# Optimization experiments

Hardware: AMD Instinct MI355X
Metric: run time of the kernel (lower is better)

The kernel has to match this reference:

```python
import jax, jax.numpy as jnp
import numpy as np

N = 100000   # nodes
E = 1600000  # edges
D_IN = 128
D = 128
G = 64       # graphs in batch
C = 2        # out_channels
EPS = 1e-5   # BatchNorm eps


def setup_inputs() -> dict:
    key = jax.random.key(0)
    ks = jax.random.split(key, 24)
    s = 0.05
    inp = {
        "x": jax.random.normal(ks[0], (N, D_IN), dtype=jnp.float32),
        "edge_index": jax.random.randint(ks[1], (2, E), 0, N, dtype=jnp.int32),
        "edge_attr": jax.random.uniform(ks[2], (E, 2), dtype=jnp.float32),
        "batch": jnp.sort(jax.random.randint(ks[3], (N,), 0, G, dtype=jnp.int32)),
        # GCN layer 0
        "Wg0": jax.random.normal(ks[4], (D_IN, D), dtype=jnp.float32) * s,
        "bg0": jnp.zeros((D,), jnp.float32),
        "gamma0": jnp.ones((D,), jnp.float32),
        "beta0": jnp.zeros((D,), jnp.float32),
        # GCN layer 1
        "Wg1": jax.random.normal(ks[5], (D, D), dtype=jnp.float32) * s,
        "bg1": jnp.zeros((D,), jnp.float32),
        "gamma1": jnp.ones((D,), jnp.float32),
        "beta1": jnp.zeros((D,), jnp.float32),
        # dense head
        "Wl1": jax.random.normal(ks[6], (D, D), dtype=jnp.float32) * s,
        "bl1": jnp.zeros((D,), jnp.float32),
        "Wl2": jax.random.normal(ks[7], (D, D), dtype=jnp.float32) * s,
        "bl2": jnp.zeros((D,), jnp.float32),
        "Wc1": jax.random.normal(ks[8], (D, D), dtype=jnp.float32) * s,
        "bc1": jnp.zeros((D,), jnp.float32),
        "Wc2": jax.random.normal(ks[9], (D, C), dtype=jnp.float32) * s,
        "bc2": jnp.zeros((C,), jnp.float32),
    }
    return inp


def _gcn_conv(x, src, dst, w, W, b):
    # PyG GCNConv: h = x @ W ; add self-loops (weight 1) ; symmetric norm ; agg at dst ; + bias
    h = x @ W                                                   # [N, D]
    deg = jax.ops.segment_sum(w, dst, num_segments=N) + 1.0     # self-loop weight 1
    dinv = jnp.where(deg > 0, jax.lax.rsqrt(deg), 0.0)          # deg^{-1/2}
    norm = dinv[src] * w * dinv[dst]                            # [E]
    agg = jax.ops.segment_sum(norm[:, None] * h[src], dst, num_segments=N)
    agg = agg + (dinv * dinv)[:, None] * h                      # self-loop contribution
    return agg + b


def _bn(x, gamma, beta):
    # training-mode batch statistics over the node dimension
    m = x.mean(axis=0)
    v = x.var(axis=0)
    return (x - m) * jax.lax.rsqrt(v + EPS) * gamma + beta


def reference(x, edge_index, edge_attr, batch,
              Wg0, bg0, gamma0, beta0,
              Wg1, bg1, gamma1, beta1,
              Wl1, bl1, Wl2, bl2, Wc1, bc1, Wc2, bc2):
    src, dst = edge_index[0], edge_index[1]
    w = edge_attr[:, 1]  # which_edge_weight is None -> column 1

    h = jax.nn.relu(_gcn_conv(x, src, dst, w, Wg0, bg0))
    h = _bn(h, gamma0, beta0)                 # dropout: identity (eval)
    h = jax.nn.relu(_gcn_conv(h, src, dst, w, Wg1, bg1))
    h = _bn(h, gamma1, beta1)

    h = jax.nn.relu(h @ Wl1 + bl1)
    h = h @ Wl2 + bl2                          # node embeddings [N, D]

    counts = jax.ops.segment_sum(jnp.ones((N,), h.dtype), batch, num_segments=G)
    graph_reps = jax.ops.segment_sum(h, batch, num_segments=G) / jnp.maximum(counts, 1.0)[:, None]

    logits = jax.nn.relu(graph_reps @ Wc1 + bc1) @ Wc2 + bc2   # [G, C]
    return (h, graph_reps, logits)
```

## Files before the change

### kernel.cpp

```cpp
#include <hip/hip_runtime.h>

#define N_NODES 100000
#define N_EDGES 1600000
#define DFEAT   128
#define NGRAPH  64
#define EPSV    1e-5f
#define SCAN_BLOCKS ((N_NODES + 255) / 256)
#define DEG_SCALE 268435456.0f
#define DEG_MASK  ((1ULL << 42) - 1)

typedef float v4f  __attribute__((ext_vector_type(4)));
typedef short v8s  __attribute__((ext_vector_type(8)));
typedef unsigned short us4 __attribute__((ext_vector_type(4)));
typedef unsigned short us8 __attribute__((ext_vector_type(8)));

static __device__ __forceinline__ unsigned short f2bf(float f) {
    union { float f; unsigned int u; } v; v.f = f;
    unsigned int u = v.u;
    return (unsigned short)((u + 0x7FFFu + ((u >> 16) & 1u)) >> 16);
}
static __device__ __forceinline__ float bf2f(unsigned short b) {
    union { unsigned int u; float f; } v; v.u = ((unsigned int)b) << 16;
    return v.f;
}

__global__ void init_kernel(unsigned long long* __restrict__ degcnt,
                            int* __restrict__ fillc, float* __restrict__ stats0,
                            float* __restrict__ stats1, float* __restrict__ gsum,
                            float* __restrict__ gcntf) {
    int i = blockIdx.x * 256 + threadIdx.x;
    if (i < N_NODES) { degcnt[i] = 0ULL; fillc[i] = 0; }
    if (i < 256)  { stats0[i] = 0.f; stats1[i] = 0.f; }
    if (i < NGRAPH * DFEAT) gsum[i] = 0.f;
    if (i < NGRAPH) gcntf[i] = 0.f;
}

__global__ __launch_bounds__(256) void wprep_kernel(
    const float* __restrict__ W0, const float* __restrict__ W1,
    const float* __restrict__ W2, const float* __restrict__ W3,
    unsigned short* __restrict__ T0, unsigned short* __restrict__ T1,
    unsigned short* __restrict__ T2, unsigned short* __restrict__ T3) {
    int which = blockIdx.x >> 6;
    int i = (blockIdx.x & 63) * 256 + threadIdx.x;
    const float* W = which == 0 ? W0 : which == 1 ? W1 : which == 2 ? W2 : W3;
    unsigned short* T = which == 0 ? T0 : which == 1 ? T1 : which == 2 ? T2 : T3;
    int n = i >> 7, k = i & 127;
    T[n * 128 + k] = f2bf(W[k * 128 + n]);
}

__global__ void edge_degcnt_kernel(const int* __restrict__ ei, const float* __restrict__ ea,
                                   unsigned long long* __restrict__ degcnt) {
    int e = blockIdx.x * 256 + threadIdx.x;
    if (e >= N_EDGES) return;
    int d = ei[N_EDGES + e];
    float w = ea[2 * e + 1];
    unsigned long long v = (1ULL << 42) | (unsigned long long)(w * DEG_SCALE);
    atomicAdd(&degcnt[d], v);
}

__global__ void dinv_kernel(const unsigned long long* __restrict__ degcnt,
                            int* __restrict__ cnt, float* __restrict__ dinv) {
    int i = blockIdx.x * 256 + threadIdx.x;
    if (i >= N_NODES) return;
    unsigned long long u = degcnt[i];
    cnt[i] = (int)(u >> 42);
    float deg = 1.0f + (float)(u & DEG_MASK) * (1.0f / DEG_SCALE);
    dinv[i] = rsqrtf(deg);
}

__global__ __launch_bounds__(256) void scan1_kernel(const int* __restrict__ cnt,
                                                    int* __restrict__ blockSum) {
    __shared__ int lds[256];
    int i = blockIdx.x * 256 + threadIdx.x;
    int t = threadIdx.x;
    lds[t] = (i < N_NODES) ? cnt[i] : 0;
    __syncthreads();
    for (int off = 128; off > 0; off >>= 1) {
        if (t < off) lds[t] += lds[t + off];
        __syncthreads();
    }
    if (t == 0) blockSum[blockIdx.x] = lds[0];
}

__global__ __launch_bounds__(512) void scan2_kernel(int* __restrict__ blockSum) {
    __shared__ int lds[512];
    int t = threadIdx.x;
    int v = (t < SCAN_BLOCKS) ? blockSum[t] : 0;
    lds[t] = v;
    __syncthreads();
    for (int off = 1; off < 512; off <<= 1) {
        int u = (t >= off) ? lds[t - off] : 0;
        __syncthreads();
        lds[t] += u;
        __syncthreads();
    }
    if (t < SCAN_BLOCKS) blockSum[t] = lds[t] - v;
}

__global__ __launch_bounds__(256) void scan3_kernel(const int* __restrict__ cnt,
                                                    const int* __restrict__ blockSum,
                                                    int* __restrict__ rowptr) {
    __shared__ int lds[256];
    int i = blockIdx.x * 256 + threadIdx.x;
    int t = threadIdx.x;
    int v = (i < N_NODES) ? cnt[i] : 0;
    lds[t] = v;
    __syncthreads();
    for (int off = 1; off < 256; off <<= 1) {
        int u = (t >= off) ? lds[t - off] : 0;
        __syncthreads();
        lds[t] += u;
        __syncthreads();
    }
    if (i < N_NODES) rowptr[i] = blockSum[blockIdx.x] + lds[t] - v;
    if (i == 0) rowptr[N_NODES] = N_EDGES;
}

__global__ void fill_kernel(const int* __restrict__ ei, const float* __restrict__ ea,
                            const float* __restrict__ dinv, const int* __restrict__ rowptr,
                            int* __restrict__ fillc, int2* __restrict__ edges) {
    int e = blockIdx.x * 256 + threadIdx.x;
    if (e >= N_EDGES) return;
    int s = ei[e], d = ei[N_EDGES + e];
    float w = ea[2 * e + 1];
    float nrm = dinv[s] * w * dinv[d];
    int pos = rowptr[d] + atomicAdd(&fillc[d], 1);
    edges[pos] = make_int2(s, __float_as_int(nrm));
}

__global__ __launch_bounds__(256) void gemm_bf16_kernel(
    const void* __restrict__ Xv, int x_is_f32,
    const unsigned short* __restrict__ Wt,
    void* __restrict__ Outv, int out_is_f32,
    const float* __restrict__ bnp, const float* __restrict__ bias, int do_relu) {
    __shared__ unsigned short Xs[128][136];
    __shared__ unsigned short Ws[128][136];
    const int tid = threadIdx.x;
    const int rb = blockIdx.x * 128;

#pragma unroll
    for (int it = 0; it < 8; ++it) {
        int flat = it * 2048 + tid * 8;
        int n = flat >> 7, k = flat & 127;
        *(us8*)&Ws[n][k] = *(const us8*)&Wt[n * 128 + k];
    }
    if (x_is_f32) {
        const float* X = (const float*)Xv;
#pragma unroll
        for (int it = 0; it < 16; ++it) {
            int flat = it * 1024 + tid * 4;
            int r = flat >> 7, k = flat & 127;
            float4 v = make_float4(0.f, 0.f, 0.f, 0.f);
            if (rb + r < N_NODES) v = *(const float4*)&X[(size_t)(rb + r) * 128 + k];
            if (bnp) {
                v.x = v.x * bnp[k]     + bnp[128 + k];
                v.y = v.y * bnp[k + 1] + bnp[129 + k];
                v.z = v.z * bnp[k + 2] + bnp[130 + k];
                v.w = v.w * bnp[k + 3] + bnp[131 + k];
            }
            us4 o; o.x = f2bf(v.x); o.y = f2bf(v.y); o.z = f2bf(v.z); o.w = f2bf(v.w);
            *(us4*)&Xs[r][k] = o;
        }
    } else {
        const unsigned short* X = (const unsigned short*)Xv;
#pragma unroll
        for (int it = 0; it < 8; ++it) {
            int flat = it * 2048 + tid * 8;
            int r = flat >> 7, k = flat & 127;
            us8 v = {0, 0, 0, 0, 0, 0, 0, 0};
            if (rb + r < N_NODES) v = *(const us8*)&X[(size_t)(rb + r) * 128 + k];
            if (bnp) {
#pragma unroll
                for (int j = 0; j < 8; ++j)
                    v[j] = f2bf(bf2f(v[j]) * bnp[k + j] + bnp[128 + k + j]);
            }
            *(us8*)&Xs[r][k] = v;
        }
    }
    __syncthreads();

    const int wv = tid >> 6, lane = tid & 63;
    const int q = lane >> 4, c16 = lane & 15;
    v4f acc[2][8];
#pragma unroll
    for (int i = 0; i < 2; ++i)
#pragma unroll
        for (int j = 0; j < 8; ++j) acc[i][j] = (v4f){0.f, 0.f, 0.f, 0.f};

#pragma unroll
    for (int ks = 0; ks < 4; ++ks) {
        v8s a0 = *(const v8s*)&Xs[wv * 32 + c16][ks * 32 + q * 8];
        v8s a1 = *(const v8s*)&Xs[wv * 32 + 16 + c16][ks * 32 + q * 8];
#pragma unroll
        for (int nt = 0; nt < 8; ++nt) {
            v8s b = *(const v8s*)&Ws[nt * 16 + c16][ks * 32 + q * 8];
            acc[0][nt] = __builtin_amdgcn_mfma_f32_16x16x32_bf16(a0, b, acc[0][nt], 0, 0, 0);
            acc[1][nt] = __builtin_amdgcn_mfma_f32_16x16x32_bf16(a1, b, acc[1][nt], 0, 0, 0);
        }
    }

#pragma unroll
    for (int mt = 0; mt < 2; ++mt) {
#pragma unroll
        for (int nt = 0; nt < 8; ++nt) {
            int col = nt * 16 + c16;
            float bcol = bias ? bias[col] : 0.f;
#pragma unroll
            for (int r = 0; r < 4; ++r) {
                int row = rb + wv * 32 + mt * 16 + q * 4 + r;
                if (row >= N_NODES) continue;
                float o = acc[mt][nt][r] + bcol;
                if (do_relu) o = fmaxf(o, 0.f);
                if (out_is_f32) ((float*)Outv)[(size_t)row * 128 + col] = o;
                else ((unsigned short*)Outv)[(size_t)row * 128 + col] = f2bf(o);
            }
        }
    }
}

__global__ __launch_bounds__(256) void agg_relu_bf16_kernel(
    const unsigned short* __restrict__ H, const int* __restrict__ rowptr,
    const int2* __restrict__ edges,
    const float* __restrict__ dinv, const float* __restrict__ bias,
    unsigned short* __restrict__ outb, float* __restrict__ stats, int nwaves) {
    __shared__ float red[1024];
    const int tid = threadIdx.x;
    const int wv = tid >> 6;
    const int lane = tid & 63;
    const float bx = bias[2 * lane], by = bias[2 * lane + 1];
    const unsigned int* __restrict__ H4 = (const unsigned int*)H;
    unsigned int* __restrict__ O4 = (unsigned int*)outb;
    float s0 = 0.f, q0 = 0.f, s1 = 0.f, q1 = 0.f;

    for (int i = blockIdx.x * 4 + wv; i < N_NODES; i += nwaves) {
        int beg = __builtin_amdgcn_readfirstlane(rowptr[i]);
        int end = __builtin_amdgcn_readfirstlane(rowptr[i + 1]);
        float px0 = 0.f, py0 = 0.f, px1 = 0.f, py1 = 0.f;
        float px2 = 0.f, py2 = 0.f, px3 = 0.f, py3 = 0.f;
        int j = beg;
        for (; j + 4 <= end; j += 4) {
            int2 e0 = edges[j], e1 = edges[j + 1], e2 = edges[j + 2], e3 = edges[j + 3];
            unsigned int h0 = H4[(size_t)e0.x * 64 + lane];
            unsigned int h1 = H4[(size_t)e1.x * 64 + lane];
            unsigned int h2 = H4[(size_t)e2.x * 64 + lane];
            unsigned int h3 = H4[(size_t)e3.x * 64 + lane];
            float v0 = __int_as_float(e0.y), v1 = __int_as_float(e1.y);
            float v2 = __int_as_float(e2.y), v3 = __int_as_float(e3.y);
            px0 = fmaf(v0, bf2f((unsigned short)h0), px0);
            py0 = fmaf(v0, bf2f((unsigned short)(h0 >> 16)), py0);
            px1 = fmaf(v1, bf2f((unsigned short)h1), px1);
            py1 = fmaf(v1, bf2f((unsigned short)(h1 >> 16)), py1);
            px2 = fmaf(v2, bf2f((unsigned short)h2), px2);
            py2 = fmaf(v2, bf2f((unsigned short)(h2 >> 16)), py2);
            px3 = fmaf(v3, bf2f((unsigned short)h3), px3);
            py3 = fmaf(v3, bf2f((unsigned short)(h3 >> 16)), py3);
        }
        for (; j < end; ++j) {
            int2 e0 = edges[j];
            float v = __int_as_float(e0.y);
            unsigned int h = H4[(size_t)e0.x * 64 + lane];
            px0 = fmaf(v, bf2f((unsigned short)h), px0);
            py0 = fmaf(v, bf2f((unsigned short)(h >> 16)), py0);
        }
        float di = dinv[i];
        float dd = di * di;
        unsigned int hs = H4[(size_t)i * 64 + lane];
        float ax = (px0 + px1) + (px2 + px3);
        float ay = (py0 + py1) + (py2 + py3);
        ax = fmaf(dd, bf2f((unsigned short)hs), ax) + bx;
        ay = fmaf(dd, bf2f((unsigned short)(hs >> 16)), ay) + by;
        ax = fmaxf(ax, 0.f);
        ay = fmaxf(ay, 0.f);
        O4[(size_t)i * 64 + lane] =
            (unsigned int)f2bf(ax) | ((unsigned int)f2bf(ay) << 16);
        s0 += ax; q0 += ax * ax; s1 += ay; q1 += ay * ay;
    }

    red[wv * 128 + 2 * lane]           = s0;
    red[wv * 128 + 2 * lane + 1]       = s1;
    red[512 + wv * 128 + 2 * lane]     = q0;
    red[512 + wv * 128 + 2 * lane + 1] = q1;
    __syncthreads();
    if (tid < 128) {
        float ts = red[tid] + red[128 + tid] + red[256 + tid] + red[384 + tid];
        float tq = red[512 + tid] + red[640 + tid] + red[768 + tid] + red[896 + tid];
        atomicAdd(&stats[tid], ts);
        atomicAdd(&stats[128 + tid], tq);
    }
}

__global__ void bn_finalize_kernel(const float* __restrict__ stats,
                                   const float* __restrict__ gamma,
                                   const float* __restrict__ beta,
                                   float* __restrict__ bnp) {
    int f = threadIdx.x;
    float mean = stats[f] / (float)N_NODES;
    float var = stats[128 + f] / (float)N_NODES - mean * mean;
    float sc = gamma[f] * rsqrtf(var + EPSV);
    bnp[f] = sc;
    bnp[128 + f] = beta[f] - mean * sc;
}

__global__ __launch_bounds__(256) void pool_kernel(const float* __restrict__ h,
                                                   const int* __restrict__ batch,
                                                   float* __restrict__ gsum,
                                                   float* __restrict__ gcntf) {
    const int f = threadIdx.x & 127;
    const int half = threadIdx.x >> 7;
    const int base = blockIdx.x * 128;
    int r = base + half;
    const int end = (base + 128 < N_NODES) ? base + 128 : N_NODES;
    if (r >= end) return;
    int cur = batch[r];
    float sum = 0.f, cnt = 0.f;
    for (; r < end; r += 2) {
        int g = batch[r];
        if (g != cur) {
            atomicAdd(&gsum[cur * 128 + f], sum);
            if (f == 0) atomicAdd(&gcntf[cur], cnt);
            sum = 0.f; cnt = 0.f; cur = g;
        }
        sum += h[(size_t)r * 128 + f];
        cnt += 1.f;
    }
    atomicAdd(&gsum[cur * 128 + f], sum);
    if (f == 0) atomicAdd(&gcntf[cur], cnt);
}

__global__ void reps_kernel(const float* __restrict__ gsum,
                            const float* __restrict__ gcntf,
                            float* __restrict__ out_reps) {
    int i = blockIdx.x * 256 + threadIdx.x;
    if (i < NGRAPH * 128) {
        int g = i >> 7;
        out_reps[i] = gsum[i] / fmaxf(gcntf[g], 1.0f);
    }
}

__global__ __launch_bounds__(128) void logits_kernel(
    const float* __restrict__ reps, const float* __restrict__ Wc1,
    const float* __restrict__ bc1, const float* __restrict__ Wc2,
    const float* __restrict__ bc2, float* __restrict__ out_logits) {
    __shared__ float repS[128];
    __shared__ float tmp[128];
    int g = blockIdx.x, t = threadIdx.x;
    repS[t] = reps[(size_t)g * 128 + t];
    __syncthreads();
    float acc = bc1[t];
    for (int k = 0; k < 128; ++k) acc = fmaf(repS[k], Wc1[k * 128 + t], acc);
    tmp[t] = fmaxf(acc, 0.f);
    __syncthreads();
    if (t < 2) {
        float a = bc2[t];
        for (int k = 0; k < 128; ++k) a = fmaf(tmp[k], Wc2[k * 2 + t], a);
        out_logits[g * 2 + t] = a;
    }
}

extern "C" void kernel_launch(void* const* d_in, const int* in_sizes, int n_in,
                              void* d_out, int out_size, void* d_ws, size_t ws_size,
                              hipStream_t stream) {
    const float* x      = (const float*)d_in[0];
    const int*   ei     = (const int*)d_in[1];
    const float* ea     = (const float*)d_in[2];
    const int*   batch  = (const int*)d_in[3];
    const float* Wg0    = (const float*)d_in[4];
    const float* bg0    = (const float*)d_in[5];
    const float* gamma0 = (const float*)d_in[6];
    const float* beta0  = (const float*)d_in[7];
    const float* Wg1    = (const float*)d_in[8];
    const float* bg1    = (const float*)d_in[9];
    const float* gamma1 = (const float*)d_in[10];
    const float* beta1  = (const float*)d_in[11];
    const float* Wl1    = (const float*)d_in[12];
    const float* bl1    = (const float*)d_in[13];
    const float* Wl2    = (const float*)d_in[14];
    const float* bl2    = (const float*)d_in[15];
    const float* Wc1    = (const float*)d_in[16];
    const float* bc1    = (const float*)d_in[17];
    const float* Wc2    = (const float*)d_in[18];
    const float* bc2    = (const float*)d_in[19];

    float* out = (float*)d_out;
    char* ws = (char*)d_ws;
    size_t off = 0;
    auto alloc = [&](size_t bytes) {
        void* p = ws + off;
        off += (bytes + 15) & ~(size_t)15;
        return p;
    };
    unsigned short* bufHb = (unsigned short*)alloc(sizeof(unsigned short) * (size_t)N_NODES * 128);
    unsigned short* bufAb = (unsigned short*)alloc(sizeof(unsigned short) * (size_t)N_NODES * 128);
    int2* edges = (int2*)alloc(sizeof(int2) * (size_t)N_EDGES);
    unsigned long long* degcnt = (unsigned long long*)alloc(sizeof(unsigned long long) * N_NODES);
    unsigned short* Wt0   = (unsigned short*)alloc(sizeof(unsigned short) * 128 * 128);
    unsigned short* Wt1   = (unsigned short*)alloc(sizeof(unsigned short) * 128 * 128);
    unsigned short* Wt2   = (unsigned short*)alloc(sizeof(unsigned short) * 128 * 128);
    unsigned short* Wt3   = (unsigned short*)alloc(sizeof(unsigned short) * 128 * 128);
    float* dinv   = (float*)alloc(sizeof(float) * N_NODES);
    int*   cnt    = (int*)alloc(sizeof(int) * N_NODES);
    int*   fillc  = (int*)alloc(sizeof(int) * N_NODES);
    float* stats0 = (float*)alloc(sizeof(float) * 256);
    float* stats1 = (float*)alloc(sizeof(float) * 256);
    float* bnp0   = (float*)alloc(sizeof(float) * 256);
    float* bnp1   = (float*)alloc(sizeof(float) * 256);
    float* gsum   = (float*)alloc(sizeof(float) * NGRAPH * 128);
    float* gcntf  = (float*)alloc(sizeof(float) * NGRAPH);
    int*   rowptr = (int*)alloc(sizeof(int) * (N_NODES + 1));
    int*   blockSum = (int*)alloc(sizeof(int) * SCAN_BLOCKS);

    init_kernel<<<(N_NODES + 255) / 256, 256, 0, stream>>>(degcnt, fillc, stats0,
                                                           stats1, gsum, gcntf);
    wprep_kernel<<<256, 256, 0, stream>>>(Wg0, Wg1, Wl1, Wl2, Wt0, Wt1, Wt2, Wt3);
    edge_degcnt_kernel<<<(N_EDGES + 255) / 256, 256, 0, stream>>>(ei, ea, degcnt);
    dinv_kernel<<<(N_NODES + 255) / 256, 256, 0, stream>>>(degcnt, cnt, dinv);
    scan1_kernel<<<SCAN_BLOCKS, 256, 0, stream>>>(cnt, blockSum);
    scan2_kernel<<<1, 512, 0, stream>>>(blockSum);
    scan3_kernel<<<SCAN_BLOCKS, 256, 0, stream>>>(cnt, blockSum, rowptr);
    fill_kernel<<<(N_EDGES + 255) / 256, 256, 0, stream>>>(ei, ea, dinv, rowptr, fillc,
                                                           edges);

    const int gemm_grid = (N_NODES + 127) / 128;
    const int agg_blocks = 2048;
    const int agg_nwaves = agg_blocks * 4;
    gemm_bf16_kernel<<<gemm_grid, 256, 0, stream>>>(x, 1, Wt0, bufHb, 0, nullptr, nullptr, 0);
    agg_relu_bf16_kernel<<<agg_blocks, 256, 0, stream>>>(bufHb, rowptr, edges,
                                                         dinv, bg0, bufAb, stats0, agg_nwaves);
    bn_finalize_kernel<<<1, 128, 0, stream>>>(stats0, gamma0, beta0, bnp0);
    gemm_bf16_kernel<<<gemm_grid, 256, 0, stream>>>(bufAb, 0, Wt1, bufHb, 0, bnp0, nullptr, 0);
    agg_relu_bf16_kernel<<<agg_blocks, 256, 0, stream>>>(bufHb, rowptr, edges,
                                                         dinv, bg1, bufAb, stats1, agg_nwaves);
    bn_finalize_kernel<<<1, 128, 0, stream>>>(stats1, gamma1, beta1, bnp1);
    gemm_bf16_kernel<<<gemm_grid, 256, 0, stream>>>(bufAb, 0, Wt2, bufHb, 0, bnp1, bl1, 1);
    gemm_bf16_kernel<<<gemm_grid, 256, 0, stream>>>(bufHb, 0, Wt3, out, 1, nullptr, bl2, 0);
    pool_kernel<<<(N_NODES + 127) / 128, 256, 0, stream>>>(out, batch, gsum, gcntf);
    reps_kernel<<<(NGRAPH * 128 + 255) / 256, 256, 0, stream>>>(
        gsum, gcntf, out + (size_t)N_NODES * 128);
    logits_kernel<<<NGRAPH, 128, 0, stream>>>(out + (size_t)N_NODES * 128, Wc1, bc1, Wc2,
                                              bc2, out + (size_t)N_NODES * 128 + NGRAPH * 128);
}
```

Measured before the change: 691.7 us.

## Slice aggregation across feature chunks with edge-parallel lanes per wave

The CSR aggregation kernel is restructured so that each block handles one 16-feature slice (eight 32-bit words) of a contiguous row range. Within a wave, eight edges are processed in parallel, each by an 8-lane group, and the partial sums are reduced with cross-lane shuffles. The aim is more memory-level parallelism per wave and better L2 locality, since the 8 slice blocks of a group share edge lists. The trade-offs are that each gather becomes a 32-byte segment instead of a full 256-byte row, the edge indices are read 8 times, and only one eighth of the lanes do the epilogue.

```diff
diff --git a/kernel.cpp b/kernel.cpp
--- a/kernel.cpp
+++ b/kernel.cpp
@@ -8,6 +8,9 @@
 #define SCAN_BLOCKS ((N_NODES + 255) / 256)
 #define DEG_SCALE 268435456.0f
 #define DEG_MASK  ((1ULL << 42) - 1)
+#define AGG_BLOCKS 4096
+#define AGG_GROUPS (AGG_BLOCKS / 8)
+#define RPB ((N_NODES + AGG_GROUPS - 1) / AGG_GROUPS)
 
 typedef float v4f  __attribute__((ext_vector_type(4)));
 typedef short v8s  __attribute__((ext_vector_type(8)));
@@ -23,6 +26,7 @@
     union { unsigned int u; float f; } v; v.u = ((unsigned int)b) << 16;
     return v.f;
 }
+static __device__ __forceinline__ int minI(int a, int b) { return a < b ? a : b; }
 
 __global__ void init_kernel(unsigned long long* __restrict__ degcnt,
                             int* __restrict__ fillc, float* __restrict__ stats0,
@@ -218,74 +222,72 @@
     }
 }
 
-__global__ __launch_bounds__(256) void agg_relu_bf16_kernel(
+__global__ __launch_bounds__(256) void agg_relu_sliced_kernel(
     const unsigned short* __restrict__ H, const int* __restrict__ rowptr,
-    const int2* __restrict__ edges,
-    const float* __restrict__ dinv, const float* __restrict__ bias,
-    unsigned short* __restrict__ outb, float* __restrict__ stats, int nwaves) {
-    __shared__ float red[1024];
+    const int2* __restrict__ edges, const float* __restrict__ dinv,
+    const float* __restrict__ bias, unsigned short* __restrict__ outb,
+    float* __restrict__ stats) {
+    const int slice = blockIdx.x & 7;
+    const int grp   = blockIdx.x >> 3;
     const int tid = threadIdx.x;
-    const int wv = tid >> 6;
-    const int lane = tid & 63;
-    const float bx = bias[2 * lane], by = bias[2 * lane + 1];
+    const int wv = tid >> 6, lane = tid & 63;
+    const int e = lane >> 3;
+    const int u = lane & 7;
+    const int ub = slice * 8 + u;
     const unsigned int* __restrict__ H4 = (const unsigned int*)H;
     unsigned int* __restrict__ O4 = (unsigned int*)outb;
+    const float bx = bias[2 * ub], by = bias[2 * ub + 1];
+
     float s0 = 0.f, q0 = 0.f, s1 = 0.f, q1 = 0.f;
-
-    for (int i = blockIdx.x * 4 + wv; i < N_NODES; i += nwaves) {
+    const int r0 = grp * RPB;
+    int r1 = r0 + RPB; if (r1 > N_NODES) r1 = N_NODES;
+
+    for (int i = r0 + wv; i < r1; i += 4) {
         int beg = __builtin_amdgcn_readfirstlane(rowptr[i]);
         int end = __builtin_amdgcn_readfirstlane(rowptr[i + 1]);
-        float px0 = 0.f, py0 = 0.f, px1 = 0.f, py1 = 0.f;
-        float px2 = 0.f, py2 = 0.f, px3 = 0.f, py3 = 0.f;
-        int j = beg;
-        for (; j + 4 <= end; j += 4) {
-            int2 e0 = edges[j], e1 = edges[j + 1], e2 = edges[j + 2], e3 = edges[j + 3];
-            unsigned int h0 = H4[(size_t)e0.x * 64 + lane];
-            unsigned int h1 = H4[(size_t)e1.x * 64 + lane];
-            unsigned int h2 = H4[(size_t)e2.x * 64 + lane];
-            unsigned int h3 = H4[(size_t)e3.x * 64 + lane];
-            float v0 = __int_as_float(e0.y), v1 = __int_as_float(e1.y);
-            float v2 = __int_as_float(e2.y), v3 = __int_as_float(e3.y);
-            px0 = fmaf(v0, bf2f((unsigned short)h0), px0);
-            py0 = fmaf(v0, bf2f((unsigned short)(h0 >> 16)), py0);
-            px1 = fmaf(v1, bf2f((unsigned short)h1), px1);
-            py1 = fmaf(v1, bf2f((unsigned short)(h1 >> 16)), py1);
-            px2 = fmaf(v2, bf2f((unsigned short)h2), px2);
-            py2 = fmaf(v2, bf2f((unsigned short)(h2 >> 16)), py2);
-            px3 = fmaf(v3, bf2f((unsigned short)h3), px3);
-            py3 = fmaf(v3, bf2f((unsigned short)(h3 >> 16)), py3);
-        }
-        for (; j < end; ++j) {
-            int2 e0 = edges[j];
-            float v = __int_as_float(e0.y);
-            unsigned int h = H4[(size_t)e0.x * 64 + lane];
-            px0 = fmaf(v, bf2f((unsigned short)h), px0);
-            py0 = fmaf(v, bf2f((unsigned short)(h >> 16)), py0);
-        }
+        int n = end - beg;
+        int last = end - 1;
         float di = dinv[i];
-        float dd = di * di;
-        unsigned int hs = H4[(size_t)i * 64 + lane];
-        float ax = (px0 + px1) + (px2 + px3);
-        float ay = (py0 + py1) + (py2 + py3);
-        ax = fmaf(dd, bf2f((unsigned short)hs), ax) + bx;
-        ay = fmaf(dd, bf2f((unsigned short)(hs >> 16)), ay) + by;
-        ax = fmaxf(ax, 0.f);
-        ay = fmaxf(ay, 0.f);
-        O4[(size_t)i * 64 + lane] =
-            (unsigned int)f2bf(ax) | ((unsigned int)f2bf(ay) << 16);
-        s0 += ax; q0 += ax * ax; s1 += ay; q1 += ay * ay;
-    }
-
-    red[wv * 128 + 2 * lane]           = s0;
-    red[wv * 128 + 2 * lane + 1]       = s1;
-    red[512 + wv * 128 + 2 * lane]     = q0;
-    red[512 + wv * 128 + 2 * lane + 1] = q1;
-    __syncthreads();
-    if (tid < 128) {
-        float ts = red[tid] + red[128 + tid] + red[256 + tid] + red[384 + tid];
-        float tq = red[512 + tid] + red[640 + tid] + red[768 + tid] + red[896 + tid];
-        atomicAdd(&stats[tid], ts);
-        atomicAdd(&stats[128 + tid], tq);
+        float ax = 0.f, ay = 0.f;
+        for (int c = 0; c < n; c += 16) {
+            int j0 = beg + c + e;
+            int j1 = j0 + 8;
+            int2 e0 = edges[minI(j0, last)];
+            int2 e1 = edges[minI(j1, last)];
+            unsigned int h0 = H4[(size_t)(unsigned)e0.x * 64 + ub];
+            unsigned int h1 = H4[(size_t)(unsigned)e1.x * 64 + ub];
+            float w0 = (c + e < n) ? __int_as_float(e0.y) : 0.f;
+            float w1 = (c + 8 + e < n) ? __int_as_float(e1.y) : 0.f;
+            ax = fmaf(w0, bf2f((unsigned short)h0), ax);
+            ay = fmaf(w0, bf2f((unsigned short)(h0 >> 16)), ay);
+            ax = fmaf(w1, bf2f((unsigned short)h1), ax);
+            ay = fmaf(w1, bf2f((unsigned short)(h1 >> 16)), ay);
+        }
+        ax += __shfl_xor(ax, 8);  ay += __shfl_xor(ay, 8);
+        ax += __shfl_xor(ax, 16); ay += __shfl_xor(ay, 16);
+        ax += __shfl_xor(ax, 32); ay += __shfl_xor(ay, 32);
+        if (e == 0) {
+            unsigned int hs = H4[(size_t)i * 64 + ub];
+            float dd = di * di;
+            ax = fmaf(dd, bf2f((unsigned short)hs), ax) + bx;
+            ay = fmaf(dd, bf2f((unsigned short)(hs >> 16)), ay) + by;
+            ax = fmaxf(ax, 0.f);
+            ay = fmaxf(ay, 0.f);
+            O4[(size_t)i * 64 + ub] =
+                (unsigned int)f2bf(ax) | ((unsigned int)f2bf(ay) << 16);
+            s0 += ax; q0 += ax * ax; s1 += ay; q1 += ay * ay;
+        }
+    }
+
+    __shared__ float red[4][8][4];
+    if (e == 0) { red[wv][u][0] = s0; red[wv][u][1] = s1;
+                  red[wv][u][2] = q0; red[wv][u][3] = q1; }
+    __syncthreads();
+    if (tid < 32) {
+        int uu = tid >> 2, v = tid & 3;
+        float t = red[0][uu][v] + red[1][uu][v] + red[2][uu][v] + red[3][uu][v];
+        int f = (slice * 8 + uu) * 2 + (v & 1);
+        atomicAdd(&stats[(v >> 1) * 128 + f], t);
     }
 }
 
@@ -421,15 +423,13 @@
                                                            edges);
 
     const int gemm_grid = (N_NODES + 127) / 128;
-    const int agg_blocks = 2048;
-    const int agg_nwaves = agg_blocks * 4;
     gemm_bf16_kernel<<<gemm_grid, 256, 0, stream>>>(x, 1, Wt0, bufHb, 0, nullptr, nullptr, 0);
-    agg_relu_bf16_kernel<<<agg_blocks, 256, 0, stream>>>(bufHb, rowptr, edges,
-                                                         dinv, bg0, bufAb, stats0, agg_nwaves);
+    agg_relu_sliced_kernel<<<AGG_BLOCKS, 256, 0, stream>>>(bufHb, rowptr, edges,
+                                                           dinv, bg0, bufAb, stats0);
     bn_finalize_kernel<<<1, 128, 0, stream>>>(stats0, gamma0, beta0, bnp0);
     gemm_bf16_kernel<<<gemm_grid, 256, 0, stream>>>(bufAb, 0, Wt1, bufHb, 0, bnp0, nullptr, 0);
-    agg_relu_bf16_kernel<<<agg_blocks, 256, 0, stream>>>(bufHb, rowptr, edges,
-                                                         dinv, bg1, bufAb, stats1, agg_nwaves);
+    agg_relu_sliced_kernel<<<AGG_BLOCKS, 256, 0, stream>>>(bufHb, rowptr, edges,
+                                                           dinv, bg1, bufAb, stats1);
     bn_finalize_kernel<<<1, 128, 0, stream>>>(stats1, gamma1, beta1, bnp1);
     gemm_bf16_kernel<<<gemm_grid, 256, 0, stream>>>(bufAb, 0, Wt2, bufHb, 0, bnp1, bl1, 1);
     gemm_bf16_kernel<<<gemm_grid, 256, 0, stream>>>(bufHb, 0, Wt3, out, 1, nullptr, bl2, 0);
```

New measurement: 955.7 us. +38.2%, slower.
